# Performance work log

Hardware: AMD Instinct MI355X
Metric: run time of the kernel (lower is better)

The kernel has to match this reference:

```python
import jax, jax.numpy as jnp
import numpy as np
from jax import lax

B, T, D, H, O = 4096, 128, 128, 150, 10

def setup_inputs() -> dict:
    key = jax.random.key(0)
    k1, k2, k3 = jax.random.split(key, 3)
    X = jax.random.normal(k1, (B, T, D), dtype=jnp.float32)
    # BasicRNNCell kernel: acts on concat([x, h]) -> [D+H, H]
    W_cell = jax.random.normal(k2, (D + H, H), dtype=jnp.float32) * (1.0 / np.sqrt(D + H))
    b_cell = jnp.zeros((H,), dtype=jnp.float32)
    W_out = jax.random.normal(k3, (H, O), dtype=jnp.float32) * (1.0 / np.sqrt(H))
    b_out = jnp.zeros((O,), dtype=jnp.float32)
    return {"X": X, "W_cell": W_cell, "b_cell": b_cell, "W_out": W_out, "b_out": b_out}

def reference(X, W_cell, b_cell, W_out, b_out):
    # dynamic_rnn with BasicRNNCell: h_t = tanh([x_t, h_{t-1}] @ W + b)
    batch = X.shape[0]
    hid = W_cell.shape[1]
    xs = jnp.swapaxes(X, 0, 1)  # [T, B, D]
    h0 = jnp.zeros((batch, hid), dtype=X.dtype)

    def step(h, x_t):
        h_new = jnp.tanh(jnp.concatenate([x_t, h], axis=-1) @ W_cell + b_cell)
        return h_new, None

    h_final, _ = lax.scan(step, h0, xs)
    # dense classifier on final state (tf code applies dense to `states`)
    logits = h_final @ W_out + b_out  # [B, O]
    return logits
```

## Files before the change

### kernel.cpp

```cpp
#include <hip/hip_runtime.h>
#include <hip/hip_bf16.h>


typedef __bf16 bf16x8 __attribute__((ext_vector_type(8)));
typedef float  f32x4  __attribute__((ext_vector_type(4)));
typedef float  f32x8  __attribute__((ext_vector_type(8)));
typedef unsigned short u16;

#define B_  4096
#define T_  128
#define D_  128
#define H_  150
#define O_  10

#define KX 4
#define KH 5
#define HPAD 168

__global__ __launch_bounds__(256, 1) void rnn_fused(
    const float* __restrict__ X,
    const float* __restrict__ Wc,
    const float* __restrict__ bc,
    const float* __restrict__ Wo,
    const float* __restrict__ bo,
    float* __restrict__ out)
{
    __shared__ __attribute__((aligned(16))) __bf16 sh_h[2][16][HPAD];

    const int tid  = threadIdx.x;
    const int wid  = tid >> 6;
    const int lane = tid & 63;
    const int q    = lane >> 4;
    const int l16  = lane & 15;
    const int row0 = blockIdx.x * 16;

    const int nt_cnt = (wid < 2) ? 3 : 2;
    const int tbase  = (wid < 2) ? wid * 3 : 6 + (wid - 2) * 2;
    const int cbase  = tbase * 16;

    {
        __bf16* p = &sh_h[0][0][0];
        for (int i = tid; i < 2 * 16 * HPAD; i += 256) p[i] = (__bf16)0.f;
    }

    bf16x8 wx[3][KX];
    bf16x8 wh[3][KH];
    float  bias[3];
    int    jc[3];
#pragma unroll
    for (int nt = 0; nt < 3; ++nt) {
        if (nt >= nt_cnt) break;
        const int  j   = (nt < 2) ? (cbase + 2 * l16 + nt) : (cbase + 32 + l16);
        const bool jv  = (j < H_);
        const int  jcl = jv ? j : 0;
        jc[nt]   = j;
        bias[nt] = jv ? bc[jcl] : 0.f;
#pragma unroll
        for (int kt = 0; kt < KX; ++kt) {
            bf16x8 f;
#pragma unroll
            for (int i = 0; i < 8; ++i) {
                const int k = kt * 32 + q * 8 + i;
                float v = Wc[k * H_ + jcl];
                v = fminf(fmaxf(v, -64.f), 64.f);
                f[i] = jv ? (__bf16)v : (__bf16)0.f;
            }
            wx[nt][kt] = f;
        }
#pragma unroll
        for (int kt = 0; kt < KH; ++kt) {
            bf16x8 f;
#pragma unroll
            for (int i = 0; i < 8; ++i) {
                const int  kh  = kt * 32 + q * 8 + i;
                const bool kv  = jv && (kh < H_);
                const int  khc = (kh < H_) ? kh : 0;
                float v = Wc[(D_ + khc) * H_ + jcl];
                v = fminf(fmaxf(v, -64.f), 64.f);
                f[i] = kv ? (__bf16)v : (__bf16)0.f;
            }
            wh[nt][kt] = f;
        }
    }

    __syncthreads();

    const float* xrow = X + (size_t)(row0 + l16) * (T_ * D_) + q * 8;

    f32x8 xb0[KX], xb1[KX];
#pragma unroll
    for (int kt = 0; kt < KX; ++kt) xb0[kt] = *(const f32x8*)(xrow + 0 * D_ + kt * 32);
#pragma unroll
    for (int kt = 0; kt < KX; ++kt) xb1[kt] = *(const f32x8*)(xrow + 1 * D_ + kt * 32);

    auto step = [&](int t, f32x8 (&xb)[KX]) {
        const __bf16 (*hb)[HPAD] = sh_h[t & 1];
        bf16x8 ah[KH];
#pragma unroll
        for (int kt = 0; kt < KH; ++kt)
            ah[kt] = *(const bf16x8*)(&hb[l16][kt * 32 + q * 8]);

        bf16x8 a[KX];
#pragma unroll
        for (int kt = 0; kt < KX; ++kt) {
#pragma unroll
            for (int i = 0; i < 8; ++i)
                a[kt][i] = (__bf16)xb[kt][i];
        }

        {
            int tt = t + 2; tt = (tt > T_ - 1) ? (T_ - 1) : tt;
#pragma unroll
            for (int kt = 0; kt < KX; ++kt)
                xb[kt] = *(const f32x8*)(xrow + (size_t)tt * D_ + kt * 32);
        }

        f32x4 ax[3], ahh[3];
#pragma unroll
        for (int nt = 0; nt < 3; ++nt) {
            if (nt >= nt_cnt) break;
            ax[nt]  = (f32x4){bias[nt], bias[nt], bias[nt], bias[nt]};
            ahh[nt] = (f32x4){0.f, 0.f, 0.f, 0.f};
        }
#pragma unroll
        for (int kt = 0; kt < KX; ++kt) {
            ax[0] = __builtin_amdgcn_mfma_f32_16x16x32_bf16(a[kt], wx[0][kt], ax[0], 0, 0, 0);
            ax[1] = __builtin_amdgcn_mfma_f32_16x16x32_bf16(a[kt], wx[1][kt], ax[1], 0, 0, 0);
            if (nt_cnt == 3)
                ax[2] = __builtin_amdgcn_mfma_f32_16x16x32_bf16(a[kt], wx[2][kt], ax[2], 0, 0, 0);
        }
#pragma unroll
        for (int kt = 0; kt < KH; ++kt) {
            ahh[0] = __builtin_amdgcn_mfma_f32_16x16x32_bf16(ah[kt], wh[0][kt], ahh[0], 0, 0, 0);
            ahh[1] = __builtin_amdgcn_mfma_f32_16x16x32_bf16(ah[kt], wh[1][kt], ahh[1], 0, 0, 0);
            if (nt_cnt == 3)
                ahh[2] = __builtin_amdgcn_mfma_f32_16x16x32_bf16(ah[kt], wh[2][kt], ahh[2], 0, 0, 0);
        }

        __bf16 (*ho)[HPAD] = sh_h[(t + 1) & 1];
#pragma unroll
        for (int r = 0; r < 4; ++r) {
            const int rr = q * 4 + r;
            const float z0 = ax[0][r] + ahh[0][r];
            const float z1 = ax[1][r] + ahh[1][r];
            const float e0 = __builtin_amdgcn_exp2f(z0 * 2.8853900817779268f);
            const float e1 = __builtin_amdgcn_exp2f(z1 * 2.8853900817779268f);
            const float h0 = 1.f - 2.f * __builtin_amdgcn_rcpf(e0 + 1.f);
            const float h1 = 1.f - 2.f * __builtin_amdgcn_rcpf(e1 + 1.f);
            const unsigned p = (unsigned)__builtin_bit_cast(u16, (__bf16)h0)
                             | ((unsigned)__builtin_bit_cast(u16, (__bf16)h1) << 16);
            *(unsigned*)(&ho[rr][cbase + 2 * l16]) = p;
            if (nt_cnt == 3) {
                const float z2 = ax[2][r] + ahh[2][r];
                const float e2 = __builtin_amdgcn_exp2f(z2 * 2.8853900817779268f);
                const float h2 = 1.f - 2.f * __builtin_amdgcn_rcpf(e2 + 1.f);
                ho[rr][cbase + 32 + l16] = (__bf16)h2;
            }
        }

        asm volatile("s_waitcnt lgkmcnt(0)\n\ts_barrier" ::: "memory");
    };

    for (int t = 0; t < T_; t += 2) {
        step(t,     xb0);
        step(t + 1, xb1);
    }

    __syncthreads();

    if (tid < 16 * O_) {
        const int row = tid / O_;
        const int o   = tid - row * O_;
        float accv = bo[o];
        const __bf16* hf = &sh_h[0][row][0];
        for (int k = 0; k < H_; ++k)
            accv += (float)hf[k] * Wo[k * O_ + o];
        out[(size_t)(row0 + row) * O_ + o] = accv;
    }
}

extern "C" void kernel_launch(void* const* d_in, const int* in_sizes, int n_in,
                              void* d_out, int out_size, void* d_ws, size_t ws_size,
                              hipStream_t stream) {
    (void)in_sizes; (void)n_in; (void)out_size; (void)d_ws; (void)ws_size;
    const float* X  = (const float*)d_in[0];
    const float* Wc = (const float*)d_in[1];
    const float* bc = (const float*)d_in[2];
    const float* Wo = (const float*)d_in[3];
    const float* bo = (const float*)d_in[4];
    rnn_fused<<<dim3(B_ / 16), dim3(256), 0, stream>>>(X, Wc, bc, Wo, bo, (float*)d_out);
}
```

Measured before the change: 434.8 us.

## Halve rows per block and stage X through a shared-memory ring buffer

Each block now handles 8 batch rows instead of 16, which doubles the grid to 512 blocks and allows two blocks per CU through launch bounds. X is loaded cooperatively as coalesced float4 per thread, converted to bf16, and kept in a 3-slot LDS ring buffer with a prefetch three steps ahead, replacing the per-lane f32x8 register prefetch. The MFMA still operates on 16 rows, with rows 8-15 duplicating rows 0-7, so half of the matrix-core work is wasted. The aim is more parallelism across CUs and fewer registers and global loads per step, at the cost of redundant MFMA work and extra LDS traffic.

```diff
diff --git a/kernel.cpp b/kernel.cpp
--- a/kernel.cpp
+++ b/kernel.cpp
@@ -3,8 +3,8 @@
 
 
 typedef __bf16 bf16x8 __attribute__((ext_vector_type(8)));
+typedef __bf16 bf16x4 __attribute__((ext_vector_type(4)));
 typedef float  f32x4  __attribute__((ext_vector_type(4)));
-typedef float  f32x8  __attribute__((ext_vector_type(8)));
 typedef unsigned short u16;
 
 #define B_  4096
@@ -16,8 +16,10 @@
 #define KX 4
 #define KH 5
 #define HPAD 168
-
-__global__ __launch_bounds__(256, 1) void rnn_fused(
+#define XPAD 136
+#define ROWS 8
+
+__global__ __launch_bounds__(256, 2) void rnn_fused(
     const float* __restrict__ X,
     const float* __restrict__ Wc,
     const float* __restrict__ bc,
@@ -25,14 +27,19 @@
     const float* __restrict__ bo,
     float* __restrict__ out)
 {
-    __shared__ __attribute__((aligned(16))) __bf16 sh_h[2][16][HPAD];
+    __shared__ __attribute__((aligned(16))) __bf16 sh_h[2][ROWS][HPAD];
+    __shared__ __attribute__((aligned(16))) __bf16 sh_x[3][ROWS][XPAD];
 
     const int tid  = threadIdx.x;
     const int wid  = tid >> 6;
     const int lane = tid & 63;
     const int q    = lane >> 4;
     const int l16  = lane & 15;
-    const int row0 = blockIdx.x * 16;
+    const int arow = l16 & 7;
+    const int row0 = blockIdx.x * ROWS;
+
+    const int srow = tid >> 5;
+    const int scol = (tid & 31) * 4;
 
     const int nt_cnt = (wid < 2) ? 3 : 2;
     const int tbase  = (wid < 2) ? wid * 3 : 6 + (wid - 2) * 2;
@@ -40,20 +47,18 @@
 
     {
         __bf16* p = &sh_h[0][0][0];
-        for (int i = tid; i < 2 * 16 * HPAD; i += 256) p[i] = (__bf16)0.f;
+        for (int i = tid; i < 2 * ROWS * HPAD; i += 256) p[i] = (__bf16)0.f;
     }
 
     bf16x8 wx[3][KX];
     bf16x8 wh[3][KH];
     float  bias[3];
-    int    jc[3];
 #pragma unroll
     for (int nt = 0; nt < 3; ++nt) {
         if (nt >= nt_cnt) break;
         const int  j   = (nt < 2) ? (cbase + 2 * l16 + nt) : (cbase + 32 + l16);
         const bool jv  = (j < H_);
         const int  jcl = jv ? j : 0;
-        jc[nt]   = j;
         bias[nt] = jv ? bc[jcl] : 0.f;
 #pragma unroll
         for (int kt = 0; kt < KX; ++kt) {
@@ -83,37 +88,33 @@
         }
     }
 
+    const float* Xg = X + (size_t)(row0 + srow) * (T_ * D_) + scol;
+#pragma unroll
+    for (int s = 0; s < 2; ++s) {
+        f32x4 v = *(const f32x4*)(Xg + (size_t)s * D_);
+        bf16x4 w;
+#pragma unroll
+        for (int i = 0; i < 4; ++i) w[i] = (__bf16)v[i];
+        *(bf16x4*)(&sh_x[s][srow][scol]) = w;
+    }
+    f32x4 xl_cur = *(const f32x4*)(Xg + (size_t)2 * D_);
+
     __syncthreads();
 
-    const float* xrow = X + (size_t)(row0 + l16) * (T_ * D_) + q * 8;
-
-    f32x8 xb0[KX], xb1[KX];
-#pragma unroll
-    for (int kt = 0; kt < KX; ++kt) xb0[kt] = *(const f32x8*)(xrow + 0 * D_ + kt * 32);
-#pragma unroll
-    for (int kt = 0; kt < KX; ++kt) xb1[kt] = *(const f32x8*)(xrow + 1 * D_ + kt * 32);
-
-    auto step = [&](int t, f32x8 (&xb)[KX]) {
-        const __bf16 (*hb)[HPAD] = sh_h[t & 1];
-        bf16x8 ah[KH];
+    int cur = 0;
+    for (int t = 0; t < T_; ++t) {
+        const int tt = (t + 3 < T_) ? (t + 3) : (T_ - 1);
+        f32x4 xl_next = *(const f32x4*)(Xg + (size_t)tt * D_);
+
+        const __bf16* xb = &sh_x[cur][0][0];
+        const __bf16* hb = &sh_h[t & 1][0][0];
+        bf16x8 a[KX], ah[KH];
+#pragma unroll
+        for (int kt = 0; kt < KX; ++kt)
+            a[kt] = *(const bf16x8*)(xb + arow * XPAD + kt * 32 + q * 8);
 #pragma unroll
         for (int kt = 0; kt < KH; ++kt)
-            ah[kt] = *(const bf16x8*)(&hb[l16][kt * 32 + q * 8]);
-
-        bf16x8 a[KX];
-#pragma unroll
-        for (int kt = 0; kt < KX; ++kt) {
-#pragma unroll
-            for (int i = 0; i < 8; ++i)
-                a[kt][i] = (__bf16)xb[kt][i];
-        }
-
-        {
-            int tt = t + 2; tt = (tt > T_ - 1) ? (T_ - 1) : tt;
-#pragma unroll
-            for (int kt = 0; kt < KX; ++kt)
-                xb[kt] = *(const f32x8*)(xrow + (size_t)tt * D_ + kt * 32);
-        }
+            ah[kt] = *(const bf16x8*)(hb + arow * HPAD + kt * 32 + q * 8);
 
         f32x4 ax[3], ahh[3];
 #pragma unroll
@@ -135,6 +136,15 @@
             ahh[1] = __builtin_amdgcn_mfma_f32_16x16x32_bf16(ah[kt], wh[1][kt], ahh[1], 0, 0, 0);
             if (nt_cnt == 3)
                 ahh[2] = __builtin_amdgcn_mfma_f32_16x16x32_bf16(ah[kt], wh[2][kt], ahh[2], 0, 0, 0);
+        }
+
+        {
+            const int wslot = (cur == 0) ? 2 : cur - 1;
+            bf16x4 w;
+#pragma unroll
+            for (int i = 0; i < 4; ++i) w[i] = (__bf16)xl_cur[i];
+            *(bf16x4*)(&sh_x[wslot][srow][scol]) = w;
+            xl_cur = xl_next;
         }
 
         __bf16 (*ho)[HPAD] = sh_h[(t + 1) & 1];
@@ -147,28 +157,29 @@
             const float e1 = __builtin_amdgcn_exp2f(z1 * 2.8853900817779268f);
             const float h0 = 1.f - 2.f * __builtin_amdgcn_rcpf(e0 + 1.f);
             const float h1 = 1.f - 2.f * __builtin_amdgcn_rcpf(e1 + 1.f);
-            const unsigned p = (unsigned)__builtin_bit_cast(u16, (__bf16)h0)
-                             | ((unsigned)__builtin_bit_cast(u16, (__bf16)h1) << 16);
-            *(unsigned*)(&ho[rr][cbase + 2 * l16]) = p;
+            float h2 = 0.f;
             if (nt_cnt == 3) {
                 const float z2 = ax[2][r] + ahh[2][r];
                 const float e2 = __builtin_amdgcn_exp2f(z2 * 2.8853900817779268f);
-                const float h2 = 1.f - 2.f * __builtin_amdgcn_rcpf(e2 + 1.f);
-                ho[rr][cbase + 32 + l16] = (__bf16)h2;
+                h2 = 1.f - 2.f * __builtin_amdgcn_rcpf(e2 + 1.f);
+            }
+            if (q < 2) {
+                const unsigned p = (unsigned)__builtin_bit_cast(u16, (__bf16)h0)
+                                 | ((unsigned)__builtin_bit_cast(u16, (__bf16)h1) << 16);
+                *(unsigned*)(&ho[rr][cbase + 2 * l16]) = p;
+                if (nt_cnt == 3)
+                    ho[rr][cbase + 32 + l16] = (__bf16)h2;
             }
         }
 
         asm volatile("s_waitcnt lgkmcnt(0)\n\ts_barrier" ::: "memory");
-    };
-
-    for (int t = 0; t < T_; t += 2) {
-        step(t,     xb0);
-        step(t + 1, xb1);
+
+        cur = (cur == 2) ? 0 : cur + 1;
     }
 
     __syncthreads();
 
-    if (tid < 16 * O_) {
+    if (tid < ROWS * O_) {
         const int row = tid / O_;
         const int o   = tid - row * O_;
         float accv = bo[o];
@@ -188,5 +199,5 @@
     const float* bc = (const float*)d_in[2];
     const float* Wo = (const float*)d_in[3];
     const float* bo = (const float*)d_in[4];
-    rnn_fused<<<dim3(B_ / 16), dim3(256), 0, stream>>>(X, Wc, bc, Wo, bo, (float*)d_out);
+    rnn_fused<<<dim3(B_ / ROWS), dim3(256), 0, stream>>>(X, Wc, bc, Wo, bo, (float*)d_out);
 }
```

Measured after the change: 417.2 us. -4.0%, faster.
